# Performance work log

Measured on AMD Instinct MI355X. Metric: run time of the kernel, lower is better.

The kernel has to match this reference:

```python
import jax, jax.numpy as jnp
import numpy as np

N_NODES = 100000
N_EDGES = 1600000
ND, ED, HD = 64, 64, 128
LN_EPS = 1e-5


def layer_norm(h, gamma, beta):
    mu = jnp.mean(h, axis=-1, keepdims=True)
    var = jnp.mean(jnp.square(h - mu), axis=-1, keepdims=True)
    return (h - mu) * jax.lax.rsqrt(var + LN_EPS) * gamma + beta


def setup_inputs() -> dict:
    key = jax.random.key(0)
    ks = jax.random.split(key, 16)
    x = jax.random.normal(ks[0], (N_NODES, ND), dtype=jnp.float32)
    edge_attr = jax.random.normal(ks[1], (N_EDGES, ED), dtype=jnp.float32)
    edge_index = jax.random.randint(ks[2], (2, N_EDGES), 0, N_NODES, dtype=jnp.int64)
    s = 0.05
    return {
        "x": x,
        "edge_attr": edge_attr,
        "edge_index": edge_index,
        "eW1": jax.random.normal(ks[3], (2 * ND + ED, HD), dtype=jnp.float32) * s,
        "eb1": jnp.zeros((HD,), dtype=jnp.float32),
        "eW2": jax.random.normal(ks[4], (HD, ED), dtype=jnp.float32) * s,
        "eb2": jnp.zeros((ED,), dtype=jnp.float32),
        "eg": jnp.ones((ED,), dtype=jnp.float32),
        "ebt": jnp.zeros((ED,), dtype=jnp.float32),
        "nW1": jax.random.normal(ks[5], (ND + ED, HD), dtype=jnp.float32) * s,
        "nb1": jnp.zeros((HD,), dtype=jnp.float32),
        "nW2": jax.random.normal(ks[6], (HD, ND), dtype=jnp.float32) * s,
        "nb2": jnp.zeros((ND,), dtype=jnp.float32),
        "ng": jnp.ones((ND,), dtype=jnp.float32),
        "nbt": jnp.zeros((ND,), dtype=jnp.float32),
    }


def reference(x, edge_attr, edge_index, eW1, eb1, eW2, eb2, eg, ebt,
              nW1, nb1, nW2, nb2, ng, nbt):
    src, dst = edge_index[0], edge_index[1]
    # edge update: gather endpoints, concat, MLP + LayerNorm, residual
    edge_input = jnp.concatenate([x[src], x[dst], edge_attr], axis=1)  # [E, 2*ND+ED]
    h = jax.nn.relu(edge_input @ eW1 + eb1)
    edge_new = layer_norm(h @ eW2 + eb2, eg, ebt)
    edge_attr = edge_attr + edge_new
    # aggregate edges into destination nodes
    edge_aggr = jax.ops.segment_sum(edge_attr, dst, num_segments=x.shape[0])  # [N, ED]
    # node update
    node_input = jnp.concatenate([x, edge_aggr], axis=1)  # [N, ND+ED]
    h = jax.nn.relu(node_input @ nW1 + nb1)
    x_new = layer_norm(h @ nW2 + nb2, ng, nbt)
    return (x + x_new, edge_attr)
```

## Files before the change

kernel.cpp:

```cpp
#include <hip/hip_runtime.h>

#define N_NODES 100000
#define N_EDGES 1600000
#define CAP 60

typedef unsigned short u16;
typedef short s16x8 __attribute__((ext_vector_type(8)));
typedef float f32x4 __attribute__((ext_vector_type(4)));
typedef unsigned u32x2 __attribute__((ext_vector_type(2)));
typedef unsigned u32x4 __attribute__((ext_vector_type(4)));

__device__ __forceinline__ u16 f2bf(float f) {
    union { float f; unsigned int i; } c;
    c.f = f;
    unsigned int u = c.i;
    return (u16)((u + 0x7fffu + ((u >> 16) & 1u)) >> 16);
}

__device__ __forceinline__ unsigned pkbf(float lo, float hi) {
    return (unsigned)f2bf(lo) | ((unsigned)f2bf(hi) << 16);
}

__device__ __forceinline__ f32x4 mfma16(s16x8 a, s16x8 b, f32x4 c) {
    return __builtin_amdgcn_mfma_f32_16x16x32_bf16(a, b, c, 0, 0, 0);
}

__global__ __launch_bounds__(256) void detect_idx(const int* __restrict__ eidx,
                                                  int* __restrict__ flag)
{
    __shared__ int snz;
    const int tid = threadIdx.x;
    if (tid == 0) snz = 0;
    __syncthreads();
    int nz = 0;
    #pragma unroll
    for (int k = 0; k < 8; ++k) {
        long pos = 1 + 2 * ((long)tid * 781 + k * 97);
        if (pos < 2L * N_EDGES) nz |= (eidx[pos] != 0);
    }
    if (nz) snz = 1;
    __syncthreads();
    if (tid == 0) *flag = snz ? 0 : 1;
}

__global__ __launch_bounds__(256) void build_csr(
    const void* __restrict__ eidx_raw, const int* __restrict__ flag64,
    int* __restrict__ cnt, int* __restrict__ idx)
{
    const long e = (long)blockIdx.x * 256 + threadIdx.x;
    if (e >= N_EDGES) return;
    const int f64 = *flag64;
    int d = f64 ? (int)((const long long*)eidx_raw)[(long)N_EDGES + e]
                : ((const int*)eidx_raw)[(long)N_EDGES + e];
    d = min(max(d, 0), N_NODES - 1);
    int slot = atomicAdd(&cnt[d], 1);
    if (slot < CAP) idx[(long)d * CAP + slot] = (int)e;
}

__global__ __launch_bounds__(256) void pack_w(
    const float* __restrict__ eW1, const float* __restrict__ eW2,
    const float* __restrict__ nW1, const float* __restrict__ nW2,
    u16* __restrict__ W1p, u16* __restrict__ W2p,
    u16* __restrict__ nW1p, u16* __restrict__ nW2p)
{
    int t = blockIdx.x * 256 + threadIdx.x;
    if (t < 24576) {
        int j = t & 7, kg = (t >> 3) & 3, n = (t >> 5) & 127, ks = t >> 12;
        W1p[t] = f2bf(eW1[(ks * 32 + kg * 8 + j) * 128 + n]);
    } else if (t < 24576 + 8192) {
        int u = t - 24576;
        int j = u & 7, kg = (u >> 3) & 3, n = (u >> 5) & 63, ks = u >> 11;
        W2p[u] = f2bf(eW2[(ks * 32 + kg * 8 + j) * 64 + n]);
    } else if (t < 24576 + 8192 + 16384) {
        int u = t - (24576 + 8192);
        int j = u & 7, kg = (u >> 3) & 3, n = (u >> 5) & 127, ks = u >> 12;
        nW1p[u] = f2bf(nW1[(ks * 32 + kg * 8 + j) * 128 + n]);
    } else if (t < 24576 + 8192 + 16384 + 8192) {
        int u = t - (24576 + 8192 + 16384);
        int j = u & 7, kg = (u >> 3) & 3, n = (u >> 5) & 63, ks = u >> 11;
        nW2p[u] = f2bf(nW2[(ks * 32 + kg * 8 + j) * 64 + n]);
    }
}

#define LDA1 200
#define LDH  136
#define LDC  68

__global__ __launch_bounds__(256, 6) void edge_kernel(
    const float* __restrict__ x, const float* __restrict__ ea,
    const void* __restrict__ eidx_raw, const int* __restrict__ flag64,
    const u16* __restrict__ W1p, const float* __restrict__ eb1,
    const u16* __restrict__ W2p, const float* __restrict__ eb2,
    const float* __restrict__ eg, const float* __restrict__ ebt,
    float* __restrict__ out_e)
{
    __shared__ __align__(16) u16 A1[64 * LDA1];
    __shared__ int s_src[64];
    __shared__ int s_dst[64];
    u16* Hs   = A1;
    float* C2 = (float*)A1;

    const int tid = threadIdx.x;
    const int lane = tid & 63;
    const int w = tid >> 6;
    const int l15 = lane & 15;
    const int l4 = lane >> 4;
    const long e0 = (long)blockIdx.x * 64;
    const int f64 = *flag64;

    const int lrow = tid >> 2;
    const int lq = tid & 3;
    const float* rp = ea + (e0 + lrow) * 64 + lq * 16;
    f32x4 rv0 = *(const f32x4*)(rp);
    f32x4 rv1 = *(const f32x4*)(rp + 4);
    f32x4 rv2 = *(const f32x4*)(rp + 8);
    f32x4 rv3 = *(const f32x4*)(rp + 12);

    if (tid < 64) {
        int v = f64 ? (int)((const long long*)eidx_raw)[e0 + tid]
                    : ((const int*)eidx_raw)[e0 + tid];
        s_src[tid] = min(max(v, 0), N_NODES - 1);
    } else if (tid < 128) {
        int t = tid - 64;
        int v = f64 ? (int)((const long long*)eidx_raw)[(long)N_EDGES + e0 + t]
                    : ((const int*)eidx_raw)[(long)N_EDGES + e0 + t];
        s_dst[t] = min(max(v, 0), N_NODES - 1);
    }
    __syncthreads();

    {
        const int s = tid & 15;
        const int cb = tid >> 4;
        #pragma unroll
        for (int p = 0; p < 8; ++p) {
            int chunk = p * 16 + cb;
            int i = chunk >> 1;
            int seg = chunk & 1;
            const float* srcp = x + (long)(seg ? s_dst[i] : s_src[i]) * 64;
            f32x4 v = *(const f32x4*)(srcp + s * 4);
            u32x2 wv;
            wv[0] = pkbf(v[0], v[1]); wv[1] = pkbf(v[2], v[3]);
            *(u32x2*)&A1[i * LDA1 + seg * 64 + s * 4] = wv;
        }
    }
    unsigned prs[8];
    prs[0] = pkbf(rv0[0], rv0[1]); prs[1] = pkbf(rv0[2], rv0[3]);
    prs[2] = pkbf(rv1[0], rv1[1]); prs[3] = pkbf(rv1[2], rv1[3]);
    prs[4] = pkbf(rv2[0], rv2[1]); prs[5] = pkbf(rv2[2], rv2[3]);
    prs[6] = pkbf(rv3[0], rv3[1]); prs[7] = pkbf(rv3[2], rv3[3]);
    {
        u16* ap = &A1[lrow * LDA1 + 128 + lq * 16];
        u32x4 w0 = {prs[0], prs[1], prs[2], prs[3]};
        u32x4 w1 = {prs[4], prs[5], prs[6], prs[7]};
        *(u32x4*)(ap) = w0;
        *(u32x4*)(ap + 8) = w1;
    }
    __syncthreads();

    s16x8 bf1[6][2];
    #pragma unroll
    for (int ks = 0; ks < 6; ++ks)
        #pragma unroll
        for (int nt = 0; nt < 2; ++nt) {
            int n = 32 * w + nt * 16 + l15;
            bf1[ks][nt] = *(const s16x8*)(W1p + ((size_t)(ks * 128 + n) * 4 + l4) * 8);
        }
    f32x4 acc[4][2] = {};
    #pragma unroll
    for (int ks = 0; ks < 6; ++ks) {
        #pragma unroll
        for (int mt = 0; mt < 4; ++mt) {
            s16x8 a = *(const s16x8*)&A1[(mt * 16 + l15) * LDA1 + ks * 32 + l4 * 8];
            #pragma unroll
            for (int nt = 0; nt < 2; ++nt)
                acc[mt][nt] = mfma16(a, bf1[ks][nt], acc[mt][nt]);
        }
    }
    __syncthreads();

    #pragma unroll
    for (int nt = 0; nt < 2; ++nt) {
        int n = 32 * w + nt * 16 + l15;
        float b = eb1[n];
        #pragma unroll
        for (int mt = 0; mt < 4; ++mt) {
            float v0 = fmaxf(acc[mt][nt][0] + b, 0.f);
            float v1 = fmaxf(acc[mt][nt][1] + b, 0.f);
            float v2 = fmaxf(acc[mt][nt][2] + b, 0.f);
            float v3 = fmaxf(acc[mt][nt][3] + b, 0.f);
            unsigned w0 = pkbf(v0, v1), w1 = pkbf(v2, v3);
            int r0 = mt * 16 + l4 * 4;
            Hs[(r0 + 0) * LDH + n] = (u16)w0;
            Hs[(r0 + 1) * LDH + n] = (u16)(w0 >> 16);
            Hs[(r0 + 2) * LDH + n] = (u16)w1;
            Hs[(r0 + 3) * LDH + n] = (u16)(w1 >> 16);
        }
    }
    __syncthreads();

    s16x8 bf2v[4];
    #pragma unroll
    for (int ks = 0; ks < 4; ++ks)
        bf2v[ks] = *(const s16x8*)(W2p + ((size_t)(ks * 64 + 16 * w + l15) * 4 + l4) * 8);
    f32x4 acc2[4] = {};
    #pragma unroll
    for (int ks = 0; ks < 4; ++ks) {
        #pragma unroll
        for (int mt = 0; mt < 4; ++mt) {
            s16x8 a = *(const s16x8*)&Hs[(mt * 16 + l15) * LDH + ks * 32 + l4 * 8];
            acc2[mt] = mfma16(a, bf2v[ks], acc2[mt]);
        }
    }
    __syncthreads();

    {
        int n = 16 * w + l15;
        float b = eb2[n];
        #pragma unroll
        for (int mt = 0; mt < 4; ++mt)
            #pragma unroll
            for (int r = 0; r < 4; ++r)
                C2[(mt * 16 + l4 * 4 + r) * LDC + n] = acc2[mt][r] + b;
    }
    __syncthreads();

    {
        const float* cp = &C2[lrow * LDC + lq * 16];
        float vv[16];
        #pragma unroll
        for (int i = 0; i < 4; ++i) {
            f32x4 t = *(const f32x4*)(cp + i * 4);
            vv[i * 4 + 0] = t[0]; vv[i * 4 + 1] = t[1];
            vv[i * 4 + 2] = t[2]; vv[i * 4 + 3] = t[3];
        }
        float s = 0.f, ss = 0.f;
        #pragma unroll
        for (int i = 0; i < 16; ++i) { s += vv[i]; ss += vv[i] * vv[i]; }
        s  += __shfl_xor(s, 1);  s  += __shfl_xor(s, 2);
        ss += __shfl_xor(ss, 1); ss += __shfl_xor(ss, 2);
        const float mu = s * (1.0f / 64.0f);
        const float var = ss * (1.0f / 64.0f) - mu * mu;
        const float rs = rsqrtf(var + 1e-5f);
        float* op = out_e + (e0 + lrow) * 64 + lq * 16;
        #pragma unroll
        for (int i4 = 0; i4 < 4; ++i4) {
            f32x4 o;
            #pragma unroll
            for (int j2 = 0; j2 < 2; ++j2) {
                union { unsigned u; float f; } lo, hi;
                lo.u = prs[i4 * 2 + j2] << 16;
                hi.u = prs[i4 * 2 + j2] & 0xffff0000u;
                const int c0 = lq * 16 + i4 * 4 + j2 * 2;
                o[j2 * 2 + 0] = (vv[i4 * 4 + j2 * 2 + 0] - mu) * rs * eg[c0] + ebt[c0] + lo.f;
                o[j2 * 2 + 1] = (vv[i4 * 4 + j2 * 2 + 1] - mu) * rs * eg[c0 + 1] + ebt[c0 + 1] + hi.f;
            }
            *(f32x4*)(op + i4 * 4) = o;
        }
    }
}

__global__ __launch_bounds__(256, 6) void node_kernel(
    const float* __restrict__ x, const float* __restrict__ out_e,
    const int* __restrict__ cnt, const int* __restrict__ idx,
    const u16* __restrict__ W1p, const float* __restrict__ nb1,
    const u16* __restrict__ W2p, const float* __restrict__ nb2,
    const float* __restrict__ ng, const float* __restrict__ nbt,
    float* __restrict__ out_x)
{
    __shared__ __align__(16) u16 A[64 * LDH];
    u16* Hs   = A;
    float* C2 = (float*)A;

    const int tid = threadIdx.x;
    const int lane = tid & 63;
    const int w = tid >> 6;
    const int l15 = lane & 15;
    const int l4 = lane >> 4;
    const int n0 = blockIdx.x * 64;

    const int lrow = tid >> 2;
    const int lq = tid & 3;
    {
        int n = n0 + lrow;
        if (n >= N_NODES) n = N_NODES - 1;
        int c = cnt[n];
        if (c > CAP) c = CAP;
        const int* ip = idx + (long)n * CAP;
        f32x4 s0 = {}, s1 = {}, s2 = {}, s3 = {};
        int j = 0;
        for (; j + 4 <= c; j += 4) {
            int ev0 = ip[j], ev1 = ip[j + 1], ev2 = ip[j + 2], ev3 = ip[j + 3];
            const float* p0 = out_e + (long)ev0 * 64 + lq * 16;
            const float* p1 = out_e + (long)ev1 * 64 + lq * 16;
            const float* p2 = out_e + (long)ev2 * 64 + lq * 16;
            const float* p3 = out_e + (long)ev3 * 64 + lq * 16;
            f32x4 a00 = *(const f32x4*)(p0);     f32x4 a01 = *(const f32x4*)(p0 + 4);
            f32x4 a02 = *(const f32x4*)(p0 + 8); f32x4 a03 = *(const f32x4*)(p0 + 12);
            f32x4 a10 = *(const f32x4*)(p1);     f32x4 a11 = *(const f32x4*)(p1 + 4);
            f32x4 a12 = *(const f32x4*)(p1 + 8); f32x4 a13 = *(const f32x4*)(p1 + 12);
            f32x4 a20 = *(const f32x4*)(p2);     f32x4 a21 = *(const f32x4*)(p2 + 4);
            f32x4 a22 = *(const f32x4*)(p2 + 8); f32x4 a23 = *(const f32x4*)(p2 + 12);
            f32x4 a30 = *(const f32x4*)(p3);     f32x4 a31 = *(const f32x4*)(p3 + 4);
            f32x4 a32 = *(const f32x4*)(p3 + 8); f32x4 a33 = *(const f32x4*)(p3 + 12);
            s0 += a00 + a10 + a20 + a30;
            s1 += a01 + a11 + a21 + a31;
            s2 += a02 + a12 + a22 + a32;
            s3 += a03 + a13 + a23 + a33;
        }
        for (; j < c; ++j) {
            int ev = ip[j];
            const float* p = out_e + (long)ev * 64 + lq * 16;
            s0 += *(const f32x4*)(p);
            s1 += *(const f32x4*)(p + 4);
            s2 += *(const f32x4*)(p + 8);
            s3 += *(const f32x4*)(p + 12);
        }
        u16* ap = &A[lrow * LDH + 64 + lq * 16];
        u32x2 o;
        o[0] = pkbf(s0[0], s0[1]); o[1] = pkbf(s0[2], s0[3]);
        *(u32x2*)(ap) = o;
        o[0] = pkbf(s1[0], s1[1]); o[1] = pkbf(s1[2], s1[3]);
        *(u32x2*)(ap + 4) = o;
        o[0] = pkbf(s2[0], s2[1]); o[1] = pkbf(s2[2], s2[3]);
        *(u32x2*)(ap + 8) = o;
        o[0] = pkbf(s3[0], s3[1]); o[1] = pkbf(s3[2], s3[3]);
        *(u32x2*)(ap + 12) = o;
    }

    {
        const int s = tid & 15;
        const int rb = tid >> 4;
        #pragma unroll
        for (int p = 0; p < 4; ++p) {
            int row = p * 16 + rb;
            long gr = n0 + row;
            if (gr >= N_NODES) gr = N_NODES - 1;
            f32x4 v = *(const f32x4*)(x + gr * 64 + s * 4);
            u32x2 o;
            o[0] = pkbf(v[0], v[1]); o[1] = pkbf(v[2], v[3]);
            *(u32x2*)&A[row * LDH + s * 4] = o;
        }
    }
    __syncthreads();

    s16x8 bf1[4][2];
    #pragma unroll
    for (int ks = 0; ks < 4; ++ks)
        #pragma unroll
        for (int nt = 0; nt < 2; ++nt) {
            int n = 32 * w + nt * 16 + l15;
            bf1[ks][nt] = *(const s16x8*)(W1p + ((size_t)(ks * 128 + n) * 4 + l4) * 8);
        }
    f32x4 acc[4][2] = {};
    #pragma unroll
    for (int ks = 0; ks < 4; ++ks) {
        #pragma unroll
        for (int mt = 0; mt < 4; ++mt) {
            s16x8 a = *(const s16x8*)&A[(mt * 16 + l15) * LDH + ks * 32 + l4 * 8];
            #pragma unroll
            for (int nt = 0; nt < 2; ++nt)
                acc[mt][nt] = mfma16(a, bf1[ks][nt], acc[mt][nt]);
        }
    }
    __syncthreads();

    #pragma unroll
    for (int nt = 0; nt < 2; ++nt) {
        int n = 32 * w + nt * 16 + l15;
        float b = nb1[n];
        #pragma unroll
        for (int mt = 0; mt < 4; ++mt) {
            float v0 = fmaxf(acc[mt][nt][0] + b, 0.f);
            float v1 = fmaxf(acc[mt][nt][1] + b, 0.f);
            float v2 = fmaxf(acc[mt][nt][2] + b, 0.f);
            float v3 = fmaxf(acc[mt][nt][3] + b, 0.f);
            unsigned w0 = pkbf(v0, v1), w1 = pkbf(v2, v3);
            int r0 = mt * 16 + l4 * 4;
            Hs[(r0 + 0) * LDH + n] = (u16)w0;
            Hs[(r0 + 1) * LDH + n] = (u16)(w0 >> 16);
            Hs[(r0 + 2) * LDH + n] = (u16)w1;
            Hs[(r0 + 3) * LDH + n] = (u16)(w1 >> 16);
        }
    }
    __syncthreads();

    s16x8 bf2v[4];
    #pragma unroll
    for (int ks = 0; ks < 4; ++ks)
        bf2v[ks] = *(const s16x8*)(W2p + ((size_t)(ks * 64 + 16 * w + l15) * 4 + l4) * 8);
    f32x4 acc2[4] = {};
    #pragma unroll
    for (int ks = 0; ks < 4; ++ks) {
        #pragma unroll
        for (int mt = 0; mt < 4; ++mt) {
            s16x8 a = *(const s16x8*)&Hs[(mt * 16 + l15) * LDH + ks * 32 + l4 * 8];
            acc2[mt] = mfma16(a, bf2v[ks], acc2[mt]);
        }
    }
    __syncthreads();

    {
        int n = 16 * w + l15;
        float b = nb2[n];
        #pragma unroll
        for (int mt = 0; mt < 4; ++mt)
            #pragma unroll
            for (int r = 0; r < 4; ++r)
                C2[(mt * 16 + l4 * 4 + r) * LDC + n] = acc2[mt][r] + b;
    }
    __syncthreads();

    {
        const float* cp = &C2[lrow * LDC + lq * 16];
        float vv[16];
        #pragma unroll
        for (int i = 0; i < 4; ++i) {
            f32x4 t = *(const f32x4*)(cp + i * 4);
            vv[i * 4 + 0] = t[0]; vv[i * 4 + 1] = t[1];
            vv[i * 4 + 2] = t[2]; vv[i * 4 + 3] = t[3];
        }
        float s = 0.f, ss = 0.f;
        #pragma unroll
        for (int i = 0; i < 16; ++i) { s += vv[i]; ss += vv[i] * vv[i]; }
        s  += __shfl_xor(s, 1);  s  += __shfl_xor(s, 2);
        ss += __shfl_xor(ss, 1); ss += __shfl_xor(ss, 2);
        const float mu = s * (1.0f / 64.0f);
        const float var = ss * (1.0f / 64.0f) - mu * mu;
        const float rs = rsqrtf(var + 1e-5f);
        const long gnode = n0 + lrow;
        if (gnode < N_NODES) {
            const float* rp = x + gnode * 64 + lq * 16;
            float* op = out_x + gnode * 64 + lq * 16;
            #pragma unroll
            for (int i4 = 0; i4 < 4; ++i4) {
                f32x4 res = *(const f32x4*)(rp + i4 * 4);
                f32x4 o;
                #pragma unroll
                for (int j = 0; j < 4; ++j) {
                    const int c = lq * 16 + i4 * 4 + j;
                    o[j] = (vv[i4 * 4 + j] - mu) * rs * ng[c] + nbt[c] + res[j];
                }
                *(f32x4*)(op + i4 * 4) = o;
            }
        }
    }
}

extern "C" void kernel_launch(void* const* d_in, const int* in_sizes, int n_in,
                              void* d_out, int out_size, void* d_ws, size_t ws_size,
                              hipStream_t stream) {
    const float* x   = (const float*)d_in[0];
    const float* ea  = (const float*)d_in[1];
    const void*  ei  = d_in[2];
    const float* eW1 = (const float*)d_in[3];
    const float* eb1 = (const float*)d_in[4];
    const float* eW2 = (const float*)d_in[5];
    const float* eb2 = (const float*)d_in[6];
    const float* eg  = (const float*)d_in[7];
    const float* ebt = (const float*)d_in[8];
    const float* nW1 = (const float*)d_in[9];
    const float* nb1 = (const float*)d_in[10];
    const float* nW2 = (const float*)d_in[11];
    const float* nb2 = (const float*)d_in[12];
    const float* ng  = (const float*)d_in[13];
    const float* nbt = (const float*)d_in[14];

    float* out   = (float*)d_out;
    float* out_x = out;
    float* out_e = out + (size_t)N_NODES * 64;

    u16* W1p   = (u16*)d_ws;
    u16* W2p   = W1p + 24576;
    u16* nW1p  = W2p + 8192;
    u16* nW2p  = nW1p + 16384;
    int* flag  = (int*)((char*)d_ws + 114688);
    int* cnt   = (int*)((char*)d_ws + 114944);
    int* idx   = (int*)((char*)d_ws + 515072);

    hipMemsetAsync(cnt, 0, (size_t)N_NODES * sizeof(int), stream);
    detect_idx<<<1, 256, 0, stream>>>((const int*)ei, flag);
    pack_w<<<224, 256, 0, stream>>>(eW1, eW2, nW1, nW2, W1p, W2p, nW1p, nW2p);
    build_csr<<<(N_EDGES + 255) / 256, 256, 0, stream>>>(ei, flag, cnt, idx);
    edge_kernel<<<N_EDGES / 64, 256, 0, stream>>>(x, ea, ei, flag, W1p, eb1,
                                                  W2p, eb2, eg, ebt, out_e);
    node_kernel<<<(N_NODES + 63) / 64, 256, 0, stream>>>(x, out_e, cnt, idx,
                                                         nW1p, nb1, nW2p, nb2,
                                                         ng, nbt, out_x);
}
```

Measured before the change: 604.2 us.

## Restructure edge kernel so each wave handles 16 edges independently

Each wave now owns its own 16 edges. It gathers the endpoint features and edge attributes straight from global memory into MFMA A-fragments in registers, skipping the shared-memory staging tile. All weight fragments are streamed from global/L2 per wave instead of being split across waves, and block-wide syncthreads become wave barriers on a per-wave LDS scratch tile. The residual now reads the original fp32 edge_attr instead of a bf16-rounded copy, which changes numerics toward the reference. The cost is reloading the full W1/W2 per wave, heavier register use, and lower occupancy (launch bounds 4 instead of 6).

```diff
diff --git a/kernel.cpp b/kernel.cpp
--- a/kernel.cpp
+++ b/kernel.cpp
@@ -82,11 +82,12 @@
     }
 }
 
-#define LDA1 200
 #define LDH  136
 #define LDC  68
-
-__global__ __launch_bounds__(256, 6) void edge_kernel(
+#define HTS  136
+#define CTS  68
+
+__global__ __launch_bounds__(256, 4) void edge_kernel(
     const float* __restrict__ x, const float* __restrict__ ea,
     const void* __restrict__ eidx_raw, const int* __restrict__ flag64,
     const u16* __restrict__ W1p, const float* __restrict__ eb1,
@@ -94,138 +95,95 @@
     const float* __restrict__ eg, const float* __restrict__ ebt,
     float* __restrict__ out_e)
 {
-    __shared__ __align__(16) u16 A1[64 * LDA1];
-    __shared__ int s_src[64];
-    __shared__ int s_dst[64];
-    u16* Hs   = A1;
-    float* C2 = (float*)A1;
+    __shared__ __align__(16) u16 HT[4][2176];
 
     const int tid = threadIdx.x;
     const int lane = tid & 63;
-    const int w = tid >> 6;
+    const int wv = tid >> 6;
     const int l15 = lane & 15;
     const int l4 = lane >> 4;
-    const long e0 = (long)blockIdx.x * 64;
+    u16* Ht = &HT[wv][0];
+    float* Ct = (float*)&HT[wv][0];
+
+    const long e0 = (long)blockIdx.x * 64 + (long)wv * 16;
     const int f64 = *flag64;
 
-    const int lrow = tid >> 2;
-    const int lq = tid & 3;
-    const float* rp = ea + (e0 + lrow) * 64 + lq * 16;
-    f32x4 rv0 = *(const f32x4*)(rp);
-    f32x4 rv1 = *(const f32x4*)(rp + 4);
-    f32x4 rv2 = *(const f32x4*)(rp + 8);
-    f32x4 rv3 = *(const f32x4*)(rp + 12);
-
-    if (tid < 64) {
-        int v = f64 ? (int)((const long long*)eidx_raw)[e0 + tid]
-                    : ((const int*)eidx_raw)[e0 + tid];
-        s_src[tid] = min(max(v, 0), N_NODES - 1);
-    } else if (tid < 128) {
-        int t = tid - 64;
-        int v = f64 ? (int)((const long long*)eidx_raw)[(long)N_EDGES + e0 + t]
-                    : ((const int*)eidx_raw)[(long)N_EDGES + e0 + t];
-        s_dst[t] = min(max(v, 0), N_NODES - 1);
-    }
-    __syncthreads();
+    const long er = e0 + l15;
+    int srcI, dstI;
+    if (f64) {
+        srcI = (int)((const long long*)eidx_raw)[er];
+        dstI = (int)((const long long*)eidx_raw)[N_EDGES + er];
+    } else {
+        srcI = ((const int*)eidx_raw)[er];
+        dstI = ((const int*)eidx_raw)[N_EDGES + er];
+    }
+    srcI = min(max(srcI, 0), N_NODES - 1);
+    dstI = min(max(dstI, 0), N_NODES - 1);
+    const float* xs  = x + (long)srcI * 64;
+    const float* xd  = x + (long)dstI * 64;
+    const float* eap = ea + er * 64;
+
+    s16x8 af[6];
+    #pragma unroll
+    for (int ks = 0; ks < 6; ++ks) {
+        const float* bp = (ks < 2 ? xs : (ks < 4 ? xd : eap)) + (ks & 1) * 32 + l4 * 8;
+        f32x4 v0 = *(const f32x4*)bp;
+        f32x4 v1 = *(const f32x4*)(bp + 4);
+        union { u32x4 u; s16x8 s; } cv;
+        cv.u[0] = pkbf(v0[0], v0[1]); cv.u[1] = pkbf(v0[2], v0[3]);
+        cv.u[2] = pkbf(v1[0], v1[1]); cv.u[3] = pkbf(v1[2], v1[3]);
+        af[ks] = cv.s;
+    }
+
+    f32x4 acc1[8] = {};
+    #pragma unroll
+    for (int ks = 0; ks < 6; ++ks) {
+        #pragma unroll
+        for (int nt = 0; nt < 8; ++nt) {
+            s16x8 b = *(const s16x8*)(W1p + ((size_t)(ks * 128 + nt * 16 + l15) * 4 + l4) * 8);
+            acc1[nt] = mfma16(af[ks], b, acc1[nt]);
+        }
+    }
+
+    #pragma unroll
+    for (int nt = 0; nt < 8; ++nt) {
+        float b = eb1[nt * 16 + l15];
+        #pragma unroll
+        for (int r = 0; r < 4; ++r) {
+            float v = fmaxf(acc1[nt][r] + b, 0.f);
+            Ht[(l4 * 4 + r) * HTS + nt * 16 + l15] = f2bf(v);
+        }
+    }
+    __builtin_amdgcn_wave_barrier();
+
+    s16x8 a2[4];
+    #pragma unroll
+    for (int ks2 = 0; ks2 < 4; ++ks2)
+        a2[ks2] = *(const s16x8*)&Ht[l15 * HTS + ks2 * 32 + l4 * 8];
+    f32x4 acc2[4] = {};
+    #pragma unroll
+    for (int ks2 = 0; ks2 < 4; ++ks2) {
+        #pragma unroll
+        for (int nt2 = 0; nt2 < 4; ++nt2) {
+            s16x8 b2 = *(const s16x8*)(W2p + ((size_t)(ks2 * 64 + nt2 * 16 + l15) * 4 + l4) * 8);
+            acc2[nt2] = mfma16(a2[ks2], b2, acc2[nt2]);
+        }
+    }
+    __builtin_amdgcn_wave_barrier();
+
+    #pragma unroll
+    for (int nt2 = 0; nt2 < 4; ++nt2) {
+        float b = eb2[nt2 * 16 + l15];
+        #pragma unroll
+        for (int r = 0; r < 4; ++r)
+            Ct[(l4 * 4 + r) * CTS + nt2 * 16 + l15] = acc2[nt2][r] + b;
+    }
+    __builtin_amdgcn_wave_barrier();
 
     {
-        const int s = tid & 15;
-        const int cb = tid >> 4;
-        #pragma unroll
-        for (int p = 0; p < 8; ++p) {
-            int chunk = p * 16 + cb;
-            int i = chunk >> 1;
-            int seg = chunk & 1;
-            const float* srcp = x + (long)(seg ? s_dst[i] : s_src[i]) * 64;
-            f32x4 v = *(const f32x4*)(srcp + s * 4);
-            u32x2 wv;
-            wv[0] = pkbf(v[0], v[1]); wv[1] = pkbf(v[2], v[3]);
-            *(u32x2*)&A1[i * LDA1 + seg * 64 + s * 4] = wv;
-        }
-    }
-    unsigned prs[8];
-    prs[0] = pkbf(rv0[0], rv0[1]); prs[1] = pkbf(rv0[2], rv0[3]);
-    prs[2] = pkbf(rv1[0], rv1[1]); prs[3] = pkbf(rv1[2], rv1[3]);
-    prs[4] = pkbf(rv2[0], rv2[1]); prs[5] = pkbf(rv2[2], rv2[3]);
-    prs[6] = pkbf(rv3[0], rv3[1]); prs[7] = pkbf(rv3[2], rv3[3]);
-    {
-        u16* ap = &A1[lrow * LDA1 + 128 + lq * 16];
-        u32x4 w0 = {prs[0], prs[1], prs[2], prs[3]};
-        u32x4 w1 = {prs[4], prs[5], prs[6], prs[7]};
-        *(u32x4*)(ap) = w0;
-        *(u32x4*)(ap + 8) = w1;
-    }
-    __syncthreads();
-
-    s16x8 bf1[6][2];
-    #pragma unroll
-    for (int ks = 0; ks < 6; ++ks)
-        #pragma unroll
-        for (int nt = 0; nt < 2; ++nt) {
-            int n = 32 * w + nt * 16 + l15;
-            bf1[ks][nt] = *(const s16x8*)(W1p + ((size_t)(ks * 128 + n) * 4 + l4) * 8);
-        }
-    f32x4 acc[4][2] = {};
-    #pragma unroll
-    for (int ks = 0; ks < 6; ++ks) {
-        #pragma unroll
-        for (int mt = 0; mt < 4; ++mt) {
-            s16x8 a = *(const s16x8*)&A1[(mt * 16 + l15) * LDA1 + ks * 32 + l4 * 8];
-            #pragma unroll
-            for (int nt = 0; nt < 2; ++nt)
-                acc[mt][nt] = mfma16(a, bf1[ks][nt], acc[mt][nt]);
-        }
-    }
-    __syncthreads();
-
-    #pragma unroll
-    for (int nt = 0; nt < 2; ++nt) {
-        int n = 32 * w + nt * 16 + l15;
-        float b = eb1[n];
-        #pragma unroll
-        for (int mt = 0; mt < 4; ++mt) {
-            float v0 = fmaxf(acc[mt][nt][0] + b, 0.f);
-            float v1 = fmaxf(acc[mt][nt][1] + b, 0.f);
-            float v2 = fmaxf(acc[mt][nt][2] + b, 0.f);
-            float v3 = fmaxf(acc[mt][nt][3] + b, 0.f);
-            unsigned w0 = pkbf(v0, v1), w1 = pkbf(v2, v3);
-            int r0 = mt * 16 + l4 * 4;
-            Hs[(r0 + 0) * LDH + n] = (u16)w0;
-            Hs[(r0 + 1) * LDH + n] = (u16)(w0 >> 16);
-            Hs[(r0 + 2) * LDH + n] = (u16)w1;
-            Hs[(r0 + 3) * LDH + n] = (u16)(w1 >> 16);
-        }
-    }
-    __syncthreads();
-
-    s16x8 bf2v[4];
-    #pragma unroll
-    for (int ks = 0; ks < 4; ++ks)
-        bf2v[ks] = *(const s16x8*)(W2p + ((size_t)(ks * 64 + 16 * w + l15) * 4 + l4) * 8);
-    f32x4 acc2[4] = {};
-    #pragma unroll
-    for (int ks = 0; ks < 4; ++ks) {
-        #pragma unroll
-        for (int mt = 0; mt < 4; ++mt) {
-            s16x8 a = *(const s16x8*)&Hs[(mt * 16 + l15) * LDH + ks * 32 + l4 * 8];
-            acc2[mt] = mfma16(a, bf2v[ks], acc2[mt]);
-        }
-    }
-    __syncthreads();
-
-    {
-        int n = 16 * w + l15;
-        float b = eb2[n];
-        #pragma unroll
-        for (int mt = 0; mt < 4; ++mt)
-            #pragma unroll
-            for (int r = 0; r < 4; ++r)
-                C2[(mt * 16 + l4 * 4 + r) * LDC + n] = acc2[mt][r] + b;
-    }
-    __syncthreads();
-
-    {
-        const float* cp = &C2[lrow * LDC + lq * 16];
+        const int row16 = lane >> 2;
+        const int q = lane & 3;
+        const float* cp = &Ct[row16 * CTS + q * 16];
         float vv[16];
         #pragma unroll
         for (int i = 0; i < 4; ++i) {
@@ -241,18 +199,17 @@
         const float mu = s * (1.0f / 64.0f);
         const float var = ss * (1.0f / 64.0f) - mu * mu;
         const float rs = rsqrtf(var + 1e-5f);
-        float* op = out_e + (e0 + lrow) * 64 + lq * 16;
+        const long eo = e0 + row16;
+        const float* rp = ea + eo * 64 + q * 16;
+        float* op = out_e + eo * 64 + q * 16;
         #pragma unroll
         for (int i4 = 0; i4 < 4; ++i4) {
+            f32x4 res = *(const f32x4*)(rp + i4 * 4);
             f32x4 o;
             #pragma unroll
-            for (int j2 = 0; j2 < 2; ++j2) {
-                union { unsigned u; float f; } lo, hi;
-                lo.u = prs[i4 * 2 + j2] << 16;
-                hi.u = prs[i4 * 2 + j2] & 0xffff0000u;
-                const int c0 = lq * 16 + i4 * 4 + j2 * 2;
-                o[j2 * 2 + 0] = (vv[i4 * 4 + j2 * 2 + 0] - mu) * rs * eg[c0] + ebt[c0] + lo.f;
-                o[j2 * 2 + 1] = (vv[i4 * 4 + j2 * 2 + 1] - mu) * rs * eg[c0 + 1] + ebt[c0 + 1] + hi.f;
+            for (int j = 0; j < 4; ++j) {
+                const int c = q * 16 + i4 * 4 + j;
+                o[j] = (vv[i4 * 4 + j] - mu) * rs * eg[c] + ebt[c] + res[j];
             }
             *(f32x4*)(op + i4 * 4) = o;
         }
```

Result: slower. 912.8 us (+51.1%).

## Persist edge blocks over four tiles with prefetch and fuse CSR build

Applied to the files above, without the earlier changes.

Each edge-kernel block now processes four 64-edge tiles in a loop. It prefetches the next tile's gathered node features and edge attributes into registers while the current tile's MLP runs, and it uses a separate LDS buffer for the hidden activations. The CSR atomics are folded into the edge kernel's index load, and the int64-detection kernel is merged into the weight-packing launch, which removes two launches. The tradeoff is lower occupancy (launch bound 6 to 3, more LDS per block) and fewer blocks in the grid.

```diff
diff --git a/kernel.cpp b/kernel.cpp
--- a/kernel.cpp
+++ b/kernel.cpp
@@ -3,6 +3,7 @@
 #define N_NODES 100000
 #define N_EDGES 1600000
 #define CAP 60
+#define T_TILES 4
 
 typedef unsigned short u16;
 typedef short s16x8 __attribute__((ext_vector_type(8)));
@@ -25,44 +26,29 @@
     return __builtin_amdgcn_mfma_f32_16x16x32_bf16(a, b, c, 0, 0, 0);
 }
 
-__global__ __launch_bounds__(256) void detect_idx(const int* __restrict__ eidx,
-                                                  int* __restrict__ flag)
-{
-    __shared__ int snz;
-    const int tid = threadIdx.x;
-    if (tid == 0) snz = 0;
-    __syncthreads();
-    int nz = 0;
-    #pragma unroll
-    for (int k = 0; k < 8; ++k) {
-        long pos = 1 + 2 * ((long)tid * 781 + k * 97);
-        if (pos < 2L * N_EDGES) nz |= (eidx[pos] != 0);
-    }
-    if (nz) snz = 1;
-    __syncthreads();
-    if (tid == 0) *flag = snz ? 0 : 1;
-}
-
-__global__ __launch_bounds__(256) void build_csr(
-    const void* __restrict__ eidx_raw, const int* __restrict__ flag64,
-    int* __restrict__ cnt, int* __restrict__ idx)
-{
-    const long e = (long)blockIdx.x * 256 + threadIdx.x;
-    if (e >= N_EDGES) return;
-    const int f64 = *flag64;
-    int d = f64 ? (int)((const long long*)eidx_raw)[(long)N_EDGES + e]
-                : ((const int*)eidx_raw)[(long)N_EDGES + e];
-    d = min(max(d, 0), N_NODES - 1);
-    int slot = atomicAdd(&cnt[d], 1);
-    if (slot < CAP) idx[(long)d * CAP + slot] = (int)e;
-}
-
 __global__ __launch_bounds__(256) void pack_w(
     const float* __restrict__ eW1, const float* __restrict__ eW2,
     const float* __restrict__ nW1, const float* __restrict__ nW2,
     u16* __restrict__ W1p, u16* __restrict__ W2p,
-    u16* __restrict__ nW1p, u16* __restrict__ nW2p)
+    u16* __restrict__ nW1p, u16* __restrict__ nW2p,
+    const int* __restrict__ eidx, int* __restrict__ flag)
 {
+    if (blockIdx.x == 224) {
+        __shared__ int snz;
+        const int tid = threadIdx.x;
+        if (tid == 0) snz = 0;
+        __syncthreads();
+        int nz = 0;
+        #pragma unroll
+        for (int k = 0; k < 8; ++k) {
+            long pos = 1 + 2 * ((long)tid * 781 + k * 97);
+            if (pos < 2L * N_EDGES) nz |= (eidx[pos] != 0);
+        }
+        if (nz) snz = 1;
+        __syncthreads();
+        if (tid == 0) *flag = snz ? 0 : 1;
+        return;
+    }
     int t = blockIdx.x * 256 + threadIdx.x;
     if (t < 24576) {
         int j = t & 7, kg = (t >> 3) & 3, n = (t >> 5) & 127, ks = t >> 12;
@@ -86,68 +72,76 @@
 #define LDH  136
 #define LDC  68
 
-__global__ __launch_bounds__(256, 6) void edge_kernel(
+__global__ __launch_bounds__(256, 3) void edge_kernel(
     const float* __restrict__ x, const float* __restrict__ ea,
     const void* __restrict__ eidx_raw, const int* __restrict__ flag64,
     const u16* __restrict__ W1p, const float* __restrict__ eb1,
     const u16* __restrict__ W2p, const float* __restrict__ eb2,
     const float* __restrict__ eg, const float* __restrict__ ebt,
-    float* __restrict__ out_e)
+    float* __restrict__ out_e, int* __restrict__ cnt, int* __restrict__ idx)
 {
     __shared__ __align__(16) u16 A1[64 * LDA1];
-    __shared__ int s_src[64];
-    __shared__ int s_dst[64];
-    u16* Hs   = A1;
-    float* C2 = (float*)A1;
+    __shared__ __align__(16) u16 B2[64 * LDH];
+    __shared__ int s_src[T_TILES][64];
+    __shared__ int s_dst[T_TILES][64];
+    u16* Hs   = B2;
+    float* C2 = (float*)B2;
 
     const int tid = threadIdx.x;
     const int lane = tid & 63;
     const int w = tid >> 6;
     const int l15 = lane & 15;
     const int l4 = lane >> 4;
-    const long e0 = (long)blockIdx.x * 64;
+    const long base = (long)blockIdx.x * (64 * T_TILES);
     const int f64 = *flag64;
-
     const int lrow = tid >> 2;
     const int lq = tid & 3;
-    const float* rp = ea + (e0 + lrow) * 64 + lq * 16;
-    f32x4 rv0 = *(const f32x4*)(rp);
-    f32x4 rv1 = *(const f32x4*)(rp + 4);
-    f32x4 rv2 = *(const f32x4*)(rp + 8);
-    f32x4 rv3 = *(const f32x4*)(rp + 12);
-
-    if (tid < 64) {
-        int v = f64 ? (int)((const long long*)eidx_raw)[e0 + tid]
-                    : ((const int*)eidx_raw)[e0 + tid];
-        s_src[tid] = min(max(v, 0), N_NODES - 1);
-    } else if (tid < 128) {
-        int t = tid - 64;
-        int v = f64 ? (int)((const long long*)eidx_raw)[(long)N_EDGES + e0 + t]
-                    : ((const int*)eidx_raw)[(long)N_EDGES + e0 + t];
-        s_dst[t] = min(max(v, 0), N_NODES - 1);
-    }
-    __syncthreads();
+    const int sgs = tid & 15;
+    const int scb = tid >> 4;
+
+    const float* rp0 = ea + (base + lrow) * 64 + lq * 16;
+    f32x4 rva = *(const f32x4*)(rp0);
+    f32x4 rvb = *(const f32x4*)(rp0 + 4);
+    f32x4 rvc = *(const f32x4*)(rp0 + 8);
+    f32x4 rvd = *(const f32x4*)(rp0 + 12);
 
     {
-        const int s = tid & 15;
-        const int cb = tid >> 4;
-        #pragma unroll
-        for (int p = 0; p < 8; ++p) {
-            int chunk = p * 16 + cb;
-            int i = chunk >> 1;
-            int seg = chunk & 1;
-            const float* srcp = x + (long)(seg ? s_dst[i] : s_src[i]) * 64;
-            f32x4 v = *(const f32x4*)(srcp + s * 4);
-            u32x2 wv;
-            wv[0] = pkbf(v[0], v[1]); wv[1] = pkbf(v[2], v[3]);
-            *(u32x2*)&A1[i * LDA1 + seg * 64 + s * 4] = wv;
-        }
-    }
-    unsigned prs[8];
-    prs[0] = pkbf(rv0[0], rv0[1]); prs[1] = pkbf(rv0[2], rv0[3]);
-    prs[2] = pkbf(rv1[0], rv1[1]); prs[3] = pkbf(rv1[2], rv1[3]);
-    prs[4] = pkbf(rv2[0], rv2[1]); prs[5] = pkbf(rv2[2], rv2[3]);
-    prs[6] = pkbf(rv3[0], rv3[1]); prs[7] = pkbf(rv3[2], rv3[3]);
+        const int tt = tid >> 6;
+        const int r = tid & 63;
+        const long ep = base + (long)tt * 64 + r;
+        int vs, vd;
+        if (f64) {
+            vs = (int)((const long long*)eidx_raw)[ep];
+            vd = (int)((const long long*)eidx_raw)[N_EDGES + ep];
+        } else {
+            vs = ((const int*)eidx_raw)[ep];
+            vd = ((const int*)eidx_raw)[N_EDGES + ep];
+        }
+        vs = min(max(vs, 0), N_NODES - 1);
+        vd = min(max(vd, 0), N_NODES - 1);
+        s_src[tt][r] = vs;
+        s_dst[tt][r] = vd;
+        int slot = atomicAdd(&cnt[vd], 1);
+        if (slot < CAP) idx[(long)vd * CAP + slot] = (int)ep;
+    }
+    __syncthreads();
+
+    #pragma unroll
+    for (int p = 0; p < 8; ++p) {
+        int chunk = p * 16 + scb;
+        int i = chunk >> 1;
+        int seg = chunk & 1;
+        const float* srcp = x + (long)(seg ? s_dst[0][i] : s_src[0][i]) * 64;
+        f32x4 v = *(const f32x4*)(srcp + sgs * 4);
+        u32x2 wv;
+        wv[0] = pkbf(v[0], v[1]); wv[1] = pkbf(v[2], v[3]);
+        *(u32x2*)&A1[i * LDA1 + seg * 64 + sgs * 4] = wv;
+    }
+    unsigned prs[8], prsN[8];
+    prs[0] = pkbf(rva[0], rva[1]); prs[1] = pkbf(rva[2], rva[3]);
+    prs[2] = pkbf(rvb[0], rvb[1]); prs[3] = pkbf(rvb[2], rvb[3]);
+    prs[4] = pkbf(rvc[0], rvc[1]); prs[5] = pkbf(rvc[2], rvc[3]);
+    prs[6] = pkbf(rvd[0], rvd[1]); prs[7] = pkbf(rvd[2], rvd[3]);
     {
         u16* ap = &A1[lrow * LDA1 + 128 + lq * 16];
         u32x4 w0 = {prs[0], prs[1], prs[2], prs[3]};
@@ -157,105 +151,151 @@
     }
     __syncthreads();
 
-    s16x8 bf1[6][2];
-    #pragma unroll
-    for (int ks = 0; ks < 6; ++ks)
+    f32x4 gx[8];
+    f32x4 rn0, rn1, rn2, rn3;
+
+    for (int t = 0; t < T_TILES; ++t) {
+        const long e0 = base + (long)t * 64;
+
+        if (t + 1 < T_TILES) {
+            #pragma unroll
+            for (int p = 0; p < 8; ++p) {
+                int chunk = p * 16 + scb;
+                int i = chunk >> 1;
+                int seg = chunk & 1;
+                gx[p] = *(const f32x4*)(x + (long)(seg ? s_dst[t + 1][i]
+                                                      : s_src[t + 1][i]) * 64 + sgs * 4);
+            }
+            const float* rpN = ea + (base + (long)(t + 1) * 64 + lrow) * 64 + lq * 16;
+            rn0 = *(const f32x4*)(rpN);
+            rn1 = *(const f32x4*)(rpN + 4);
+            rn2 = *(const f32x4*)(rpN + 8);
+            rn3 = *(const f32x4*)(rpN + 12);
+        }
+
+        s16x8 bf1[6][2];
+        #pragma unroll
+        for (int ks = 0; ks < 6; ++ks)
+            #pragma unroll
+            for (int nt = 0; nt < 2; ++nt) {
+                int n = 32 * w + nt * 16 + l15;
+                bf1[ks][nt] = *(const s16x8*)(W1p + ((size_t)(ks * 128 + n) * 4 + l4) * 8);
+            }
+        f32x4 acc[4][2] = {};
+        #pragma unroll
+        for (int ks = 0; ks < 6; ++ks) {
+            #pragma unroll
+            for (int mt = 0; mt < 4; ++mt) {
+                s16x8 a = *(const s16x8*)&A1[(mt * 16 + l15) * LDA1 + ks * 32 + l4 * 8];
+                #pragma unroll
+                for (int nt = 0; nt < 2; ++nt)
+                    acc[mt][nt] = mfma16(a, bf1[ks][nt], acc[mt][nt]);
+            }
+        }
+        __syncthreads();
+
         #pragma unroll
         for (int nt = 0; nt < 2; ++nt) {
             int n = 32 * w + nt * 16 + l15;
-            bf1[ks][nt] = *(const s16x8*)(W1p + ((size_t)(ks * 128 + n) * 4 + l4) * 8);
-        }
-    f32x4 acc[4][2] = {};
-    #pragma unroll
-    for (int ks = 0; ks < 6; ++ks) {
-        #pragma unroll
-        for (int mt = 0; mt < 4; ++mt) {
-            s16x8 a = *(const s16x8*)&A1[(mt * 16 + l15) * LDA1 + ks * 32 + l4 * 8];
-            #pragma unroll
-            for (int nt = 0; nt < 2; ++nt)
-                acc[mt][nt] = mfma16(a, bf1[ks][nt], acc[mt][nt]);
-        }
-    }
-    __syncthreads();
-
-    #pragma unroll
-    for (int nt = 0; nt < 2; ++nt) {
-        int n = 32 * w + nt * 16 + l15;
-        float b = eb1[n];
-        #pragma unroll
-        for (int mt = 0; mt < 4; ++mt) {
-            float v0 = fmaxf(acc[mt][nt][0] + b, 0.f);
-            float v1 = fmaxf(acc[mt][nt][1] + b, 0.f);
-            float v2 = fmaxf(acc[mt][nt][2] + b, 0.f);
-            float v3 = fmaxf(acc[mt][nt][3] + b, 0.f);
-            unsigned w0 = pkbf(v0, v1), w1 = pkbf(v2, v3);
-            int r0 = mt * 16 + l4 * 4;
-            Hs[(r0 + 0) * LDH + n] = (u16)w0;
-            Hs[(r0 + 1) * LDH + n] = (u16)(w0 >> 16);
-            Hs[(r0 + 2) * LDH + n] = (u16)w1;
-            Hs[(r0 + 3) * LDH + n] = (u16)(w1 >> 16);
-        }
-    }
-    __syncthreads();
-
-    s16x8 bf2v[4];
-    #pragma unroll
-    for (int ks = 0; ks < 4; ++ks)
-        bf2v[ks] = *(const s16x8*)(W2p + ((size_t)(ks * 64 + 16 * w + l15) * 4 + l4) * 8);
-    f32x4 acc2[4] = {};
-    #pragma unroll
-    for (int ks = 0; ks < 4; ++ks) {
-        #pragma unroll
-        for (int mt = 0; mt < 4; ++mt) {
-            s16x8 a = *(const s16x8*)&Hs[(mt * 16 + l15) * LDH + ks * 32 + l4 * 8];
-            acc2[mt] = mfma16(a, bf2v[ks], acc2[mt]);
-        }
-    }
-    __syncthreads();
-
-    {
-        int n = 16 * w + l15;
-        float b = eb2[n];
-        #pragma unroll
-        for (int mt = 0; mt < 4; ++mt)
-            #pragma unroll
-            for (int r = 0; r < 4; ++r)
-                C2[(mt * 16 + l4 * 4 + r) * LDC + n] = acc2[mt][r] + b;
-    }
-    __syncthreads();
-
-    {
-        const float* cp = &C2[lrow * LDC + lq * 16];
-        float vv[16];
-        #pragma unroll
-        for (int i = 0; i < 4; ++i) {
-            f32x4 t = *(const f32x4*)(cp + i * 4);
-            vv[i * 4 + 0] = t[0]; vv[i * 4 + 1] = t[1];
-            vv[i * 4 + 2] = t[2]; vv[i * 4 + 3] = t[3];
-        }
-        float s = 0.f, ss = 0.f;
-        #pragma unroll
-        for (int i = 0; i < 16; ++i) { s += vv[i]; ss += vv[i] * vv[i]; }
-        s  += __shfl_xor(s, 1);  s  += __shfl_xor(s, 2);
-        ss += __shfl_xor(ss, 1); ss += __shfl_xor(ss, 2);
-        const float mu = s * (1.0f / 64.0f);
-        const float var = ss * (1.0f / 64.0f) - mu * mu;
-        const float rs = rsqrtf(var + 1e-5f);
-        float* op = out_e + (e0 + lrow) * 64 + lq * 16;
-        #pragma unroll
-        for (int i4 = 0; i4 < 4; ++i4) {
-            f32x4 o;
-            #pragma unroll
-            for (int j2 = 0; j2 < 2; ++j2) {
-                union { unsigned u; float f; } lo, hi;
-                lo.u = prs[i4 * 2 + j2] << 16;
-                hi.u = prs[i4 * 2 + j2] & 0xffff0000u;
-                const int c0 = lq * 16 + i4 * 4 + j2 * 2;
-                o[j2 * 2 + 0] = (vv[i4 * 4 + j2 * 2 + 0] - mu) * rs * eg[c0] + ebt[c0] + lo.f;
-                o[j2 * 2 + 1] = (vv[i4 * 4 + j2 * 2 + 1] - mu) * rs * eg[c0 + 1] + ebt[c0 + 1] + hi.f;
-            }
-            *(f32x4*)(op + i4 * 4) = o;
-        }
+            float b = eb1[n];
+            #pragma unroll
+            for (int mt = 0; mt < 4; ++mt) {
+                float v0 = fmaxf(acc[mt][nt][0] + b, 0.f);
+                float v1 = fmaxf(acc[mt][nt][1] + b, 0.f);
+                float v2 = fmaxf(acc[mt][nt][2] + b, 0.f);
+                float v3 = fmaxf(acc[mt][nt][3] + b, 0.f);
+                unsigned w0 = pkbf(v0, v1), w1 = pkbf(v2, v3);
+                int r0 = mt * 16 + l4 * 4;
+                Hs[(r0 + 0) * LDH + n] = (u16)w0;
+                Hs[(r0 + 1) * LDH + n] = (u16)(w0 >> 16);
+                Hs[(r0 + 2) * LDH + n] = (u16)w1;
+                Hs[(r0 + 3) * LDH + n] = (u16)(w1 >> 16);
+            }
+        }
+
+        if (t + 1 < T_TILES) {
+            #pragma unroll
+            for (int p = 0; p < 8; ++p) {
+                int chunk = p * 16 + scb;
+                int i = chunk >> 1;
+                int seg = chunk & 1;
+                u32x2 wv;
+                wv[0] = pkbf(gx[p][0], gx[p][1]); wv[1] = pkbf(gx[p][2], gx[p][3]);
+                *(u32x2*)&A1[i * LDA1 + seg * 64 + sgs * 4] = wv;
+            }
+            prsN[0] = pkbf(rn0[0], rn0[1]); prsN[1] = pkbf(rn0[2], rn0[3]);
+            prsN[2] = pkbf(rn1[0], rn1[1]); prsN[3] = pkbf(rn1[2], rn1[3]);
+            prsN[4] = pkbf(rn2[0], rn2[1]); prsN[5] = pkbf(rn2[2], rn2[3]);
+            prsN[6] = pkbf(rn3[0], rn3[1]); prsN[7] = pkbf(rn3[2], rn3[3]);
+            u16* ap = &A1[lrow * LDA1 + 128 + lq * 16];
+            u32x4 w0 = {prsN[0], prsN[1], prsN[2], prsN[3]};
+            u32x4 w1 = {prsN[4], prsN[5], prsN[6], prsN[7]};
+            *(u32x4*)(ap) = w0;
+            *(u32x4*)(ap + 8) = w1;
+        }
+        __syncthreads();
+
+        s16x8 bf2v[4];
+        #pragma unroll
+        for (int ks = 0; ks < 4; ++ks)
+            bf2v[ks] = *(const s16x8*)(W2p + ((size_t)(ks * 64 + 16 * w + l15) * 4 + l4) * 8);
+        f32x4 acc2[4] = {};
+        #pragma unroll
+        for (int ks = 0; ks < 4; ++ks) {
+            #pragma unroll
+            for (int mt = 0; mt < 4; ++mt) {
+                s16x8 a = *(const s16x8*)&Hs[(mt * 16 + l15) * LDH + ks * 32 + l4 * 8];
+                acc2[mt] = mfma16(a, bf2v[ks], acc2[mt]);
+            }
+        }
+        __syncthreads();
+
+        {
+            int n = 16 * w + l15;
+            float b = eb2[n];
+            #pragma unroll
+            for (int mt = 0; mt < 4; ++mt)
+                #pragma unroll
+                for (int r = 0; r < 4; ++r)
+                    C2[(mt * 16 + l4 * 4 + r) * LDC + n] = acc2[mt][r] + b;
+        }
+        __syncthreads();
+
+        {
+            const float* cp = &C2[lrow * LDC + lq * 16];
+            float vv[16];
+            #pragma unroll
+            for (int i = 0; i < 4; ++i) {
+                f32x4 tv = *(const f32x4*)(cp + i * 4);
+                vv[i * 4 + 0] = tv[0]; vv[i * 4 + 1] = tv[1];
+                vv[i * 4 + 2] = tv[2]; vv[i * 4 + 3] = tv[3];
+            }
+            float s = 0.f, ss = 0.f;
+            #pragma unroll
+            for (int i = 0; i < 16; ++i) { s += vv[i]; ss += vv[i] * vv[i]; }
+            s  += __shfl_xor(s, 1);  s  += __shfl_xor(s, 2);
+            ss += __shfl_xor(ss, 1); ss += __shfl_xor(ss, 2);
+            const float mu = s * (1.0f / 64.0f);
+            const float var = ss * (1.0f / 64.0f) - mu * mu;
+            const float rs = rsqrtf(var + 1e-5f);
+            float* op = out_e + (e0 + lrow) * 64 + lq * 16;
+            #pragma unroll
+            for (int i4 = 0; i4 < 4; ++i4) {
+                f32x4 o;
+                #pragma unroll
+                for (int j2 = 0; j2 < 2; ++j2) {
+                    union { unsigned u; float f; } lo, hi;
+                    lo.u = prs[i4 * 2 + j2] << 16;
+                    hi.u = prs[i4 * 2 + j2] & 0xffff0000u;
+                    const int c0 = lq * 16 + i4 * 4 + j2 * 2;
+                    o[j2 * 2 + 0] = (vv[i4 * 4 + j2 * 2 + 0] - mu) * rs * eg[c0] + ebt[c0] + lo.f;
+                    o[j2 * 2 + 1] = (vv[i4 * 4 + j2 * 2 + 1] - mu) * rs * eg[c0 + 1] + ebt[c0 + 1] + hi.f;
+                }
+                *(f32x4*)(op + i4 * 4) = o;
+            }
+        }
+        #pragma unroll
+        for (int i = 0; i < 8; ++i) prs[i] = prsN[i];
     }
 }
 
@@ -478,11 +518,10 @@
     int* idx   = (int*)((char*)d_ws + 515072);
 
     hipMemsetAsync(cnt, 0, (size_t)N_NODES * sizeof(int), stream);
-    detect_idx<<<1, 256, 0, stream>>>((const int*)ei, flag);
-    pack_w<<<224, 256, 0, stream>>>(eW1, eW2, nW1, nW2, W1p, W2p, nW1p, nW2p);
-    build_csr<<<(N_EDGES + 255) / 256, 256, 0, stream>>>(ei, flag, cnt, idx);
-    edge_kernel<<<N_EDGES / 64, 256, 0, stream>>>(x, ea, ei, flag, W1p, eb1,
-                                                  W2p, eb2, eg, ebt, out_e);
+    pack_w<<<225, 256, 0, stream>>>(eW1, eW2, nW1, nW2, W1p, W2p, nW1p, nW2p,
+                                    (const int*)ei, flag);
+    edge_kernel<<<N_EDGES / (64 * T_TILES), 256, 0, stream>>>(
+        x, ea, ei, flag, W1p, eb1, W2p, eb2, eg, ebt, out_e, cnt, idx);
     node_kernel<<<(N_NODES + 63) / 64, 256, 0, stream>>>(x, out_e, cnt, idx,
                                                          nW1p, nb1, nW2p, nb2,
                                                          ng, nbt, out_x);
```

New measurement: 861.0 us. +42.5%, slower.
